# Performance work log

Measured on AMD Instinct MI355X. Metric: run time of the kernel, lower is better.

The kernel has to match this reference:

```python
import jax, jax.numpy as jnp
import numpy as np

B = 4
S = 1024          # per-sequence length (equal for all sequences)
HQ = 32           # query heads
HK = 8            # kv heads (GQA)
D = 128           # head dim


def setup_inputs() -> dict:
    key = jax.random.key(0)
    k1, k2, k3 = jax.random.split(key, 3)
    total = B * S
    q = jax.random.normal(k1, (total, HQ, D), dtype=jnp.float32)
    k = jax.random.normal(k2, (total, HK, D), dtype=jnp.float32)
    v = jax.random.normal(k3, (total, HK, D), dtype=jnp.float32)
    cu = (jnp.arange(B + 1, dtype=jnp.int32) * S)
    return {
        "q": q, "k": k, "v": v,
        "cu_seqlens_q": cu, "cu_seqlens_k": cu,
        "max_seqlen_q": S, "max_seqlen_k": S,
    }


def reference(q, k, v, cu_seqlens_q, cu_seqlens_k, max_seqlen_q, max_seqlen_k):
    # Varlen causal GQA attention (prefill path of Attention.forward).
    # All sequences have equal length S = max_seqlen_q, so the packed varlen
    # layout is exactly a reshape to (B, S, H, D) -- same math as the
    # per-sequence Python loop in attention_varlen_func.
    total, Hq, Dh = q.shape
    Hk = k.shape[1]
    g = Hq // Hk                      # GQA group size
    Sq = int(max_seqlen_q)
    Bn = total // Sq
    scale = 1.0 / (Dh ** 0.5)

    qb = q.reshape(Bn, Sq, Hk, g, Dh)  # (B,S,Hk,g,D)
    kb = k.reshape(Bn, Sq, Hk, Dh)     # (B,S,Hk,D)
    vb = v.reshape(Bn, Sq, Hk, Dh)

    scores = jnp.einsum('bqhgd,bkhd->bhgqk', qb, kb) * scale  # (B,Hk,g,S,S)
    causal_mask = jnp.triu(jnp.ones((Sq, Sq), dtype=bool), k=1)
    scores = jnp.where(causal_mask, -jnp.inf, scores)
    attn = jax.nn.softmax(scores, axis=-1)
    out = jnp.einsum('bhgqk,bkhd->bqhgd', attn, vb)           # (B,S,Hk,g,D)
    return out.reshape(total, Hq, Dh)
```

## Files before the change

kernel.cpp:

```cpp
#include <hip/hip_runtime.h>
#include <hip/hip_bf16.h>


typedef __bf16 v8bf __attribute__((ext_vector_type(8)));
typedef __bf16 v4bf __attribute__((ext_vector_type(4)));
typedef float  v16f __attribute__((ext_vector_type(16)));

#define NB  4
#define NS  1024
#define NHQ 32
#define NHK 8
#define ND  128
#define BQ  128
#define BK  64
#define KP  136

#define KOFF(r) (16*((r)>>3) + ((((r)>>2)&1)*4) + ((r)&3))

__global__ __launch_bounds__(256, 2)
void fattn(const float* __restrict__ qg, const float* __restrict__ kg,
           const float* __restrict__ vg, float* __restrict__ og)
{
  __shared__ __align__(16) __bf16 Ks[2][BK * KP];
  __shared__ __align__(16) __bf16 Vt[2][ND * BK];
  __shared__ __align__(16) float  alq[4 * 32];

  const int tid  = threadIdx.x;
  const int lane = tid & 63;
  const int wave = tid >> 6;
  const int half = lane >> 5;
  const int l31  = lane & 31;

  const int bx = blockIdx.x;
  const int hk = bx & 7;
  const int t6 = bx >> 3;
  const int b  = t6 >> 4;
  const int m6 = t6 & 15;
  const int p  = m6 >> 2;
  const int h  = hk * 4 + (m6 & 3);

  const float scale = 0.08838834764831845f;
  const size_t kvbase = (size_t)(b * NS) * (NHK * ND) + (size_t)hk * ND;

  const int rbase = tid >> 5;
  const int kd4   = (tid & 31) << 2;
  const int vdg   = tid & 31;
  const int vkq   = tid >> 5;

  float4 pk[8];
  float4 pvf[8];
  auto prefetch = [&](int kn) {
    #pragma unroll
    for (int i = 0; i < 8; ++i)
      pk[i] = *(const float4*)(kg + kvbase + (size_t)(kn + rbase + 8 * i) * (NHK * ND) + kd4);
    const float* vp = vg + kvbase + (size_t)(kn + vkq * 8) * (NHK * ND) + 4 * vdg;
    #pragma unroll
    for (int kk = 0; kk < 8; ++kk)
      pvf[kk] = *(const float4*)(vp + (size_t)kk * (NHK * ND));
  };

  prefetch(0);
  int cur = 0;

  for (int ph = 0; ph < 2; ++ph) {
    const int qt = ph ? (7 - p) : p;
    const int wv = ph ? (3 - wave) : wave;
    const int q0 = qt * BQ;
    const int wqb = q0 + wv * 32;
    const int qglob = wqb + l31;
    const int ntiles = 2 * (qt + 1);

    v8bf qf[8];
    {
      const float* qp = qg + ((size_t)((b * NS + qglob) * NHQ + h)) * ND + half * 8;
      #pragma unroll
      for (int dM = 0; dM < 8; ++dM) {
        float4 f0 = *(const float4*)(qp + dM * 16);
        float4 f1 = *(const float4*)(qp + dM * 16 + 4);
        v8bf t;
        t[0]=(__bf16)(f0.x*scale); t[1]=(__bf16)(f0.y*scale);
        t[2]=(__bf16)(f0.z*scale); t[3]=(__bf16)(f0.w*scale);
        t[4]=(__bf16)(f1.x*scale); t[5]=(__bf16)(f1.y*scale);
        t[6]=(__bf16)(f1.z*scale); t[7]=(__bf16)(f1.w*scale);
        qf[dM] = t;
      }
    }

    v16f accO[4];
    #pragma unroll
    for (int dt = 0; dt < 4; ++dt)
      #pragma unroll
      for (int e = 0; e < 16; ++e) accO[dt][e] = 0.f;
    float m_run = -INFINITY, l_run = 0.f;

    for (int t = 0; t < ntiles; ++t) {
      const int k0 = t * BK;
      __bf16* ksb = &Ks[cur][0];
      __bf16* vtb = &Vt[cur][0];

      #pragma unroll
      for (int i = 0; i < 8; ++i) {
        int row = rbase + 8 * i;
        int o = row & 31;
        int slot = (row >> 5) * 32 + (o & 3) + 4 * ((o >> 3) & 1)
                 + 8 * (2 * (o >> 4) + ((o >> 2) & 1));
        v4bf kb;
        kb[0]=(__bf16)pk[i].x; kb[1]=(__bf16)pk[i].y;
        kb[2]=(__bf16)pk[i].z; kb[3]=(__bf16)pk[i].w;
        *(v4bf*)(&ksb[slot * KP + kd4]) = kb;
      }
      #pragma unroll
      for (int j = 0; j < 4; ++j) {
        int d = 4 * vdg + j;
        v8bf w;
        #pragma unroll
        for (int e = 0; e < 8; ++e) w[e] = (__bf16)(((const float*)&pvf[e])[j]);
        *(v8bf*)(&vtb[(d * 8 + (vkq ^ (vdg & 7))) * 8]) = w;
      }

      __syncthreads();

      if (t + 1 < ntiles)      prefetch(k0 + BK);
      else if (ph == 0)        prefetch(0);

      if (k0 <= wqb + 31) {
        const __bf16* ksr = &Ks[cur][0];
        const __bf16* vtr = &Vt[cur][0];
        v16f s0, s1;
        #pragma unroll
        for (int e = 0; e < 16; ++e) { s0[e] = 0.f; s1[e] = 0.f; }
        __builtin_amdgcn_s_setprio(1);
        #pragma unroll
        for (int dM = 0; dM < 8; ++dM) {
          v8bf ka = *(const v8bf*)(&ksr[(0 * 32 + l31) * KP + dM * 16 + half * 8]);
          s0 = __builtin_amdgcn_mfma_f32_32x32x16_bf16(ka, qf[dM], s0, 0, 0, 0);
        }
        #pragma unroll
        for (int dM = 0; dM < 8; ++dM) {
          v8bf ka = *(const v8bf*)(&ksr[(1 * 32 + l31) * KP + dM * 16 + half * 8]);
          s1 = __builtin_amdgcn_mfma_f32_32x32x16_bf16(ka, qf[dM], s1, 0, 0, 0);
        }
        __builtin_amdgcn_s_setprio(0);
        if (k0 + BK > wqb) {
          #pragma unroll
          for (int r = 0; r < 16; ++r) {
            int key = k0 + KOFF(r) + half * 8;
            if (key > qglob)      s0[r] = -INFINITY;
            if (key + 32 > qglob) s1[r] = -INFINITY;
          }
        }
        float m0 = s0[0];
        #pragma unroll
        for (int r = 1; r < 16; ++r) m0 = fmaxf(m0, s0[r]);
        #pragma unroll
        for (int r = 0; r < 16; ++r) m0 = fmaxf(m0, s1[r]);
        m0 = fmaxf(m0, __shfl_xor(m0, 32));
        float mn = fmaxf(m_run, m0);
        float rs = 0.f;
        #pragma unroll
        for (int r = 0; r < 16; ++r) { float pp = __expf(s0[r] - mn); s0[r] = pp; rs += pp; }
        #pragma unroll
        for (int r = 0; r < 16; ++r) { float pp = __expf(s1[r] - mn); s1[r] = pp; rs += pp; }
        rs += __shfl_xor(rs, 32);
        if (__any(m0 > m_run)) {
          float al = __expf(m_run - mn);
          if (half == 0) alq[wave * 32 + l31] = al;
          float4 alf[4];
          #pragma unroll
          for (int c = 0; c < 4; ++c)
            alf[c] = *(const float4*)(&alq[wave * 32 + 8 * c + 4 * half]);
          #pragma unroll
          for (int dt = 0; dt < 4; ++dt)
            #pragma unroll
            for (int r = 0; r < 16; ++r)
              accO[dt][r] *= ((const float*)&alf[r >> 2])[r & 3];
          l_run = l_run * al + rs;
        } else {
          l_run += rs;
        }
        m_run = mn;
        __builtin_amdgcn_s_setprio(1);
        #pragma unroll
        for (int C = 0; C < 2; ++C) {
          #pragma unroll
          for (int cp = 0; cp < 2; ++cp) {
            v8bf pf;
            #pragma unroll
            for (int e = 0; e < 8; ++e)
              pf[e] = (__bf16)(C == 0 ? s0[cp * 8 + e] : s1[cp * 8 + e]);
            int g = (C * 2 + cp) * 2 + half;
            #pragma unroll
            for (int dt = 0; dt < 4; ++dt) {
              int d = dt * 32 + l31;
              v8bf vb = *(const v8bf*)(&vtr[(d * 8 + (g ^ ((l31 >> 2) & 7))) * 8]);
              accO[dt] = __builtin_amdgcn_mfma_f32_32x32x16_bf16(pf, vb, accO[dt], 0, 0, 0);
            }
          }
        }
        __builtin_amdgcn_s_setprio(0);
      }
      cur ^= 1;
    }

    if (half == 0) alq[wave * 32 + l31] = 1.f / l_run;
    float4 invf[4];
    #pragma unroll
    for (int c = 0; c < 4; ++c)
      invf[c] = *(const float4*)(&alq[wave * 32 + 8 * c + 4 * half]);
    #pragma unroll
    for (int dt = 0; dt < 4; ++dt) {
      #pragma unroll
      for (int r = 0; r < 16; ++r) {
        int qrow = (r & 3) + 8 * (r >> 2) + 4 * half;
        float* op = og + ((size_t)((b * NS + wqb + qrow) * NHQ + h)) * ND;
        op[dt * 32 + l31] = accO[dt][r] * ((const float*)&invf[r >> 2])[r & 3];
      }
    }
  }
}

extern "C" void kernel_launch(void* const* d_in, const int* in_sizes, int n_in,
                              void* d_out, int out_size, void* d_ws, size_t ws_size,
                              hipStream_t stream) {
  const float* q = (const float*)d_in[0];
  const float* k = (const float*)d_in[1];
  const float* v = (const float*)d_in[2];
  float* out = (float*)d_out;
  dim3 grid(NB * NHQ * 4);
  fattn<<<grid, 256, 0, stream>>>(q, k, v, out);
}
```

Baseline: 204.6 us.

## Pre-convert K/V to swizzled bf16 tiles and DMA them directly into LDS

A new prep kernel converts K and V once to bf16 in a pre-swizzled per-tile layout in workspace. The attention kernel then fetches each 32KB tile with global_load_lds straight into shared memory, replacing per-block fp32 loads, conversions and register-staged LDS stores. The goal is to remove the redundant conversion across the four query heads sharing a KV head and to halve global traffic, at the cost of an extra launch and a workspace round-trip. The XOR swizzle replaces the padded K layout to avoid bank conflicts.

```diff
diff --git a/kernel.cpp b/kernel.cpp
--- a/kernel.cpp
+++ b/kernel.cpp
@@ -1,5 +1,6 @@
 #include <hip/hip_runtime.h>
 #include <hip/hip_bf16.h>
+#include <stdint.h>
 
 
 typedef __bf16 v8bf __attribute__((ext_vector_type(8)));
@@ -13,17 +14,58 @@
 #define ND  128
 #define BQ  128
 #define BK  64
-#define KP  136
 
 #define KOFF(r) (16*((r)>>3) + ((((r)>>2)&1)*4) + ((r)&3))
 
+__device__ __forceinline__ int kslot(int row) {
+  int o = row & 31;
+  return (row >> 5) * 32 + (o & 3) + 4 * ((o >> 3) & 1)
+       + 8 * (2 * (o >> 4) + ((o >> 2) & 1));
+}
+
+__global__ __launch_bounds__(256)
+void prep(const float* __restrict__ kg, const float* __restrict__ vg,
+          char* __restrict__ ws)
+{
+  const int tid = threadIdx.x;
+  const int blk = blockIdx.x;
+  if (blk < 4096) {
+    int gid = blk * 256 + tid;
+    int i  = gid & 31;
+    int s  = (gid >> 5) & (NS - 1);
+    int hk = (gid >> 15) & 7;
+    int b  = gid >> 18;
+    float4 f = *(const float4*)(kg + ((size_t)((b * NS + s) * NHK + hk)) * ND + 4 * i);
+    v4bf kb;
+    kb[0]=(__bf16)f.x; kb[1]=(__bf16)f.y; kb[2]=(__bf16)f.z; kb[3]=(__bf16)f.w;
+    int t = s >> 6, row = s & 63;
+    int slot = kslot(row);
+    int byte = (slot * 256 + 8 * i) ^ ((slot & 7) << 4);
+    size_t tb = (size_t)((b * 8 + hk) * 16 + t) << 15;
+    *(v4bf*)(ws + tb + byte) = kb;
+  } else {
+    int vid = (blk - 4096) * 256 + tid;
+    int d  = vid & 127;
+    int g  = (vid >> 7) & 7;
+    int t  = (vid >> 10) & 15;
+    int hk = (vid >> 14) & 7;
+    int b  = vid >> 17;
+    const float* vp = vg + ((size_t)((b * NS + t * 64 + g * 8) * NHK + hk)) * ND + d;
+    v8bf w;
+    #pragma unroll
+    for (int e = 0; e < 8; ++e) w[e] = (__bf16)vp[(size_t)e * (NHK * ND)];
+    int byte = (d * 8 + (g ^ ((d >> 2) & 7))) * 16;
+    size_t tb = (size_t)((b * 8 + hk) * 16 + t) << 15;
+    *(v8bf*)(ws + tb + 16384 + byte) = w;
+  }
+}
+
 __global__ __launch_bounds__(256, 2)
-void fattn(const float* __restrict__ qg, const float* __restrict__ kg,
-           const float* __restrict__ vg, float* __restrict__ og)
+void fattn(const float* __restrict__ qg, const char* __restrict__ kvg,
+           float* __restrict__ og)
 {
-  __shared__ __align__(16) __bf16 Ks[2][BK * KP];
-  __shared__ __align__(16) __bf16 Vt[2][ND * BK];
-  __shared__ __align__(16) float  alq[4 * 32];
+  __shared__ __align__(16) char  KV[2][32768];
+  __shared__ __align__(16) float alq[4 * 32];
 
   const int tid  = threadIdx.x;
   const int lane = tid & 63;
@@ -40,26 +82,21 @@
   const int h  = hk * 4 + (m6 & 3);
 
   const float scale = 0.08838834764831845f;
-  const size_t kvbase = (size_t)(b * NS) * (NHK * ND) + (size_t)hk * ND;
-
-  const int rbase = tid >> 5;
-  const int kd4   = (tid & 31) << 2;
-  const int vdg   = tid & 31;
-  const int vkq   = tid >> 5;
-
-  float4 pk[8];
-  float4 pvf[8];
-  auto prefetch = [&](int kn) {
-    #pragma unroll
-    for (int i = 0; i < 8; ++i)
-      pk[i] = *(const float4*)(kg + kvbase + (size_t)(kn + rbase + 8 * i) * (NHK * ND) + kd4);
-    const float* vp = vg + kvbase + (size_t)(kn + vkq * 8) * (NHK * ND) + 4 * vdg;
-    #pragma unroll
-    for (int kk = 0; kk < 8; ++kk)
-      pvf[kk] = *(const float4*)(vp + (size_t)kk * (NHK * ND));
+  const int kvtile = (b * 8 + hk) * 16;
+
+  auto dma = [&](int t_, char* dst) {
+    const char* src = kvg + ((size_t)(kvtile + t_) << 15);
+    #pragma unroll
+    for (int i = 0; i < 8; ++i) {
+      int c = wave * 8 + i;
+      __builtin_amdgcn_global_load_lds(
+        (const __attribute__((address_space(1))) void*)(src + c * 1024 + lane * 16),
+        (__attribute__((address_space(3))) void*)(dst + c * 1024),
+        16, 0, 0);
+    }
   };
 
-  prefetch(0);
+  dma(0, KV[0]);
   int cur = 0;
 
   for (int ph = 0; ph < 2; ++ph) {
@@ -95,49 +132,29 @@
 
     for (int t = 0; t < ntiles; ++t) {
       const int k0 = t * BK;
-      __bf16* ksb = &Ks[cur][0];
-      __bf16* vtb = &Vt[cur][0];
-
-      #pragma unroll
-      for (int i = 0; i < 8; ++i) {
-        int row = rbase + 8 * i;
-        int o = row & 31;
-        int slot = (row >> 5) * 32 + (o & 3) + 4 * ((o >> 3) & 1)
-                 + 8 * (2 * (o >> 4) + ((o >> 2) & 1));
-        v4bf kb;
-        kb[0]=(__bf16)pk[i].x; kb[1]=(__bf16)pk[i].y;
-        kb[2]=(__bf16)pk[i].z; kb[3]=(__bf16)pk[i].w;
-        *(v4bf*)(&ksb[slot * KP + kd4]) = kb;
-      }
-      #pragma unroll
-      for (int j = 0; j < 4; ++j) {
-        int d = 4 * vdg + j;
-        v8bf w;
-        #pragma unroll
-        for (int e = 0; e < 8; ++e) w[e] = (__bf16)(((const float*)&pvf[e])[j]);
-        *(v8bf*)(&vtb[(d * 8 + (vkq ^ (vdg & 7))) * 8]) = w;
-      }
-
+
+      asm volatile("s_waitcnt vmcnt(0)" ::: "memory");
       __syncthreads();
 
-      if (t + 1 < ntiles)      prefetch(k0 + BK);
-      else if (ph == 0)        prefetch(0);
+      if (t + 1 < ntiles)      dma(t + 1, KV[cur ^ 1]);
+      else if (ph == 0)        dma(0, KV[cur ^ 1]);
 
       if (k0 <= wqb + 31) {
-        const __bf16* ksr = &Ks[cur][0];
-        const __bf16* vtr = &Vt[cur][0];
+        const char* ksr = KV[cur];
+        const char* vtr = KV[cur] + 16384;
         v16f s0, s1;
         #pragma unroll
         for (int e = 0; e < 16; ++e) { s0[e] = 0.f; s1[e] = 0.f; }
+        const int kxor = (l31 & 7) << 4;
         __builtin_amdgcn_s_setprio(1);
         #pragma unroll
         for (int dM = 0; dM < 8; ++dM) {
-          v8bf ka = *(const v8bf*)(&ksr[(0 * 32 + l31) * KP + dM * 16 + half * 8]);
+          v8bf ka = *(const v8bf*)(ksr + ((l31 * 256 + dM * 32 + half * 16) ^ kxor));
           s0 = __builtin_amdgcn_mfma_f32_32x32x16_bf16(ka, qf[dM], s0, 0, 0, 0);
         }
         #pragma unroll
         for (int dM = 0; dM < 8; ++dM) {
-          v8bf ka = *(const v8bf*)(&ksr[(1 * 32 + l31) * KP + dM * 16 + half * 8]);
+          v8bf ka = *(const v8bf*)(ksr + (((32 + l31) * 256 + dM * 32 + half * 16) ^ kxor));
           s1 = __builtin_amdgcn_mfma_f32_32x32x16_bf16(ka, qf[dM], s1, 0, 0, 0);
         }
         __builtin_amdgcn_s_setprio(0);
@@ -192,7 +209,7 @@
             #pragma unroll
             for (int dt = 0; dt < 4; ++dt) {
               int d = dt * 32 + l31;
-              v8bf vb = *(const v8bf*)(&vtr[(d * 8 + (g ^ ((l31 >> 2) & 7))) * 8]);
+              v8bf vb = *(const v8bf*)(vtr + (d * 8 + (g ^ ((l31 >> 2) & 7))) * 16);
               accO[dt] = __builtin_amdgcn_mfma_f32_32x32x16_bf16(pf, vb, accO[dt], 0, 0, 0);
             }
           }
@@ -226,6 +243,7 @@
   const float* k = (const float*)d_in[1];
   const float* v = (const float*)d_in[2];
   float* out = (float*)d_out;
-  dim3 grid(NB * NHQ * 4);
-  fattn<<<grid, 256, 0, stream>>>(q, k, v, out);
-}
+  char* ws = (char*)d_ws;
+  prep<<<dim3(4096 + 2048), 256, 0, stream>>>(k, v, ws);
+  fattn<<<dim3(NB * NHQ * 4), 256, 0, stream>>>(q, ws, out);
+}
```

New measurement: 190.7 us. 1.07x faster.
